# Kernel optimization log

Measured on AMD Instinct MI355X. Metric: run time of the kernel, lower is better.

Reference implementation:

```python
import jax, jax.numpy as jnp
import numpy as np

B, H, W, DIM, NH = 4, 32, 32, 768, 12
HD = DIM // NH  # head_dim = 64


def setup_inputs() -> dict:
    key = jax.random.key(0)
    ks = jax.random.split(key, 12)
    n = lambda i, shape, s=1.0: jax.random.normal(ks[i], shape, jnp.float32) * s
    return {
        "q": n(0, (B, H, W, DIM)),
        "k": n(1, (B, H, W, DIM)),
        "v": n(2, (B, H, W, DIM)),
        # Linear weights stored as (in, out) so y = x @ W + b (equivalent to torch x @ W.T)
        "Wq": n(3, (DIM, DIM), 0.02), "bq": jnp.zeros((DIM,), jnp.float32),
        "Wk": n(4, (DIM, DIM), 0.02), "bk": jnp.zeros((DIM,), jnp.float32),
        "Wv": n(5, (DIM, DIM), 0.02), "bv": jnp.zeros((DIM,), jnp.float32),
        "Wp": n(6, (DIM, DIM), 0.02), "bp": jnp.zeros((DIM,), jnp.float32),
        # decomposed relative position tables: (2*size - 1, head_dim)
        "rel_pos_h": n(7, (2 * H - 1, HD), 0.02),
        "rel_pos_w": n(8, (2 * W - 1, HD), 0.02),
    }


def reference(q, k, v, Wq, bq, Wk, bk, Wv, bv, Wp, bp, rel_pos_h, rel_pos_w):
    scale = HD ** -0.5

    def to_heads(x, Wt, b):
        y = x.reshape(B, H * W, DIM) @ Wt + b          # (B, HW, DIM)
        return y.reshape(B, H * W, NH, HD).transpose(0, 2, 1, 3).reshape(B * NH, H * W, HD)

    qh = to_heads(q, Wq, bq)   # (B*NH, HW, HD)
    kh = to_heads(k, Wk, bk)
    vh = to_heads(v, Wv, bv)

    # scaled dot-product scores
    attn = jnp.einsum('bqd,bkd->bqk', qh * scale, kh)  # (B*NH, HW, HW)

    # decomposed relative position bias (q_size == k_size == input_size, no interpolation)
    idx_h = jnp.arange(H)[:, None] - jnp.arange(H)[None, :] + (H - 1)
    idx_w = jnp.arange(W)[:, None] - jnp.arange(W)[None, :] + (W - 1)
    Rh = rel_pos_h[idx_h]  # (H, H, HD)
    Rw = rel_pos_w[idx_w]  # (W, W, HD)
    rq = qh.reshape(B * NH, H, W, HD)  # unscaled q, as in torch add_decomposed_rel_pos
    rel_h = jnp.einsum('bhwc,hkc->bhwk', rq, Rh)  # (B*NH, H, W, H)
    rel_w = jnp.einsum('bhwc,wkc->bhwk', rq, Rw)  # (B*NH, H, W, W)

    attn = (attn.reshape(B * NH, H, W, H, W)
            + rel_h[:, :, :, :, None]
            + rel_w[:, :, :, None, :]).reshape(B * NH, H * W, H * W)

    attn = jax.nn.softmax(attn, axis=-1)
    x = (attn @ vh).reshape(B, NH, H, W, HD).transpose(0, 2, 3, 1, 4).reshape(B, H, W, DIM)
    return x @ Wp + bp
```

## Files before the change

### kernel.cpp

```cpp
#include <hip/hip_runtime.h>
#include <math.h>

#define DIM  768
#define NH   12
#define HD   64
#define HWN  1024
#define MROWS 4096

typedef __attribute__((ext_vector_type(8))) short short8;
typedef __attribute__((ext_vector_type(4))) float f32x4;
typedef _Float16 h8 __attribute__((ext_vector_type(8)));
typedef _Float16 h2 __attribute__((ext_vector_type(2)));

__device__ __forceinline__ void gl_lds16(const void* g, void* l) {
    __builtin_amdgcn_global_load_lds(
        (const __attribute__((address_space(1))) void*)g,
        (__attribute__((address_space(3))) void*)l, 16, 0, 0);
}

__global__ __launch_bounds__(256) void xconv_kernel(
    const float* __restrict__ q, const float* __restrict__ k,
    const float* __restrict__ v, _Float16* __restrict__ xf16)
{
    const int N8 = MROWS * DIM / 8;
    int i = blockIdx.x * 256 + threadIdx.x;
    const int stride = gridDim.x * 256;
    for (; i < 3 * N8; i += stride) {
        const int sel = i / N8, j = i - sel * N8;
        const float* src = (sel == 0) ? q : (sel == 1) ? k : v;
        float4 a0 = ((const float4*)src)[j * 2];
        float4 a1 = ((const float4*)src)[j * 2 + 1];
        h8 o = {(_Float16)a0.x, (_Float16)a0.y, (_Float16)a0.z, (_Float16)a0.w,
                (_Float16)a1.x, (_Float16)a1.y, (_Float16)a1.z, (_Float16)a1.w};
        *(h8*)(xf16 + (size_t)sel * (MROWS * DIM) + (size_t)j * 8) = o;
    }
}

__global__ __launch_bounds__(256) void wconv_kernel(
    const float* __restrict__ Wq, const float* __restrict__ Wk,
    const float* __restrict__ Wv, const float* __restrict__ Wp,
    _Float16* __restrict__ WtAll)
{
    __shared__ float Ws[64][65];
    const int z = blockIdx.z;
    const float* W = (z == 0) ? Wq : (z == 1) ? Wk : (z == 2) ? Wv : Wp;
    _Float16* Wt = WtAll + (size_t)z * 589824;

    const int k0 = blockIdx.y * 64, n0 = blockIdx.x * 64;
    const int t = threadIdx.x;
    {
        int r = t >> 2, c4 = (t & 3) * 16;
        #pragma unroll
        for (int u = 0; u < 16; u += 4)
            *(float4*)&Ws[r][c4 + u] = *(const float4*)(W + (size_t)(k0 + r) * DIM + n0 + c4 + u);
    }
    __syncthreads();
    const int n = t >> 2, kseg = (t & 3) * 16;
    h8 h0, h1;
    #pragma unroll
    for (int j = 0; j < 8; ++j) {
        h0[j] = (_Float16)Ws[kseg + j][n];
        h1[j] = (_Float16)Ws[kseg + 8 + j][n];
    }
    size_t base = (size_t)(n0 + n) * DIM + k0 + kseg;
    *(h8*)(Wt + base) = h0;
    *(h8*)(Wt + base + 8) = h1;
}

__global__ __launch_bounds__(256) void rel2frag_kernel(
    const float* __restrict__ rph, const float* __restrict__ rpw,
    _Float16* __restrict__ relTg)
{
    const int t = threadIdx.x;
    const int row = t >> 1, c0 = (t & 1) * 32;
    const float* src = (row < 63) ? rph + (size_t)row * HD
                     : (row >= 64 && row < 127) ? rpw + (size_t)(row - 64) * HD
                     : nullptr;
    #pragma unroll
    for (int g = 0; g < 4; ++g) {
        h8 o;
        #pragma unroll
        for (int j = 0; j < 8; ++j)
            o[j] = src ? (_Float16)src[c0 + g * 8 + j] : (_Float16)0.0f;
        *(h8*)(relTg + (size_t)row * HD + c0 + g * 8) = o;
    }
}

template<int AMODE>
__global__ __launch_bounds__(256, 3) void gemm_mfma_kernel(
    const _Float16* __restrict__ X0, const _Float16* __restrict__ WtAll,
    const float* __restrict__ bias0, const float* __restrict__ bias1,
    const float* __restrict__ bias2,
    void* __restrict__ Y0, void* __restrict__ Y1, void* __restrict__ Y2)
{
    constexpr int NT  = (AMODE == 0) ? 128 : 64;
    constexpr int NBF = NT / 16;
    constexpr int WCF = NT / 32;
    __shared__ __align__(16) char smem[16384 + 2 * NBF * 1024];
    constexpr int BOFF = 16384;

    const int t = threadIdx.x;
    const int w = t >> 6, lane = t & 63;
    const int l15 = lane & 15, l4 = lane >> 4;

    int sel, rem, rb, cb;
    if (AMODE == 0) {
        const int sw = (blockIdx.x & 7) * 72 + (blockIdx.x >> 3);
        sel = sw / 192; rem = sw - sel * 192;
        rb = rem / 6; cb = rem - rb * 6;
    } else {
        const int sw = (blockIdx.x & 7) * 48 + (blockIdx.x >> 3);
        sel = 3; rem = sw;
        rb = rem / 12; cb = rem - rb * 12;
    }
    const int row0 = rb * 128, col0 = cb * NT;

    const char* Ab = (const char*)(X0 + (AMODE == 0 ? (size_t)sel * (MROWS * DIM) : 0));
    const _Float16* Bt = WtAll + (size_t)sel * 589824;
    const float* bias = (AMODE == 1) ? bias0 : (sel == 0) ? bias0 : (sel == 1) ? bias1 : bias2;

    f32x4 acc[4][WCF];
    #pragma unroll
    for (int i = 0; i < 4; ++i)
        #pragma unroll
        for (int j = 0; j < WCF; ++j) acc[i][j] = (f32x4){0, 0, 0, 0};

    for (int kt = 0; kt < 12; ++kt) {
        #pragma unroll
        for (int i = 0; i < 4; ++i) {
            const int fi = w * 4 + i;
            const int row = fi * 8 + (lane >> 3);
            const int srcb = ((lane & 7) * 16) ^ ((row & 7) << 4);
            gl_lds16(Ab + (size_t)(row0 + row) * 1536 + kt * 128 + srcb, smem + fi * 1024);
        }
        #pragma unroll
        for (int it = 0; it < 2 * NBF / 4; ++it) {
            const int f = it * 4 + w;
            const int ks = f / NBF, cf = f % NBF;
            const size_t off = (size_t)(col0 + cf * 16 + l15) * 1536 + kt * 128 + ks * 64 + l4 * 16;
            gl_lds16((const char*)Bt + off, smem + BOFF + f * 1024);
        }
        __syncthreads();

        __builtin_amdgcn_s_setprio(1);
        #pragma unroll
        for (int ks = 0; ks < 2; ++ks) {
            h8 b[WCF];
            #pragma unroll
            for (int cf4 = 0; cf4 < WCF; ++cf4) {
                const int fb = ks * NBF + (w & 1) * WCF + cf4;
                b[cf4] = *(const h8*)(smem + BOFF + fb * 1024 + lane * 16);
            }
            #pragma unroll
            for (int rf = 0; rf < 4; ++rf) {
                const int arow = (w >> 1) * 64 + rf * 16 + l15;
                const int base = arow * 128 + ((ks * 64 + l4 * 16) ^ ((arow & 7) << 4));
                h8 ah = *(const h8*)(smem + base);
                #pragma unroll
                for (int cf4 = 0; cf4 < WCF; ++cf4)
                    acc[rf][cf4] = __builtin_amdgcn_mfma_f32_16x16x32_f16(ah, b[cf4], acc[rf][cf4], 0, 0, 0);
            }
        }
        __builtin_amdgcn_s_setprio(0);
        __syncthreads();
    }

    const int wrow0 = row0 + (w >> 1) * 64;
    const int wcol0 = col0 + (w & 1) * (WCF * 16);
    #pragma unroll
    for (int cf4 = 0; cf4 < WCF; ++cf4) {
        const int c = wcol0 + cf4 * 16 + l15;
        const float bb = bias[c - (AMODE == 0 ? 0 : col0) + (AMODE == 0 ? 0 : col0)];
        #pragma unroll
        for (int rf = 0; rf < 4; ++rf) {
            #pragma unroll
            for (int reg = 0; reg < 4; ++reg) {
                const int r = wrow0 + rf * 16 + l4 * 4 + reg;
                float y = acc[rf][cf4][reg] + bb;
                if (AMODE == 1) {
                    ((float*)Y0)[(size_t)r * DIM + c] = y;
                } else {
                    _Float16* Yh = (_Float16*)((sel == 0) ? Y0 : (sel == 1) ? Y1 : Y2);
                    size_t base = ((size_t)((r >> 10) * NH + (c >> 6)) * HWN + (r & 1023)) * HD + (c & 63);
                    Yh[base] = (_Float16)y;
                }
            }
        }
    }
}

#define AT_REL   0
#define AT_VT    8704
#define AT_P     25088
#define AT_KB    33280
#define AT_QF    8704
#define AT_RELT  17920
#define AT_PG    17920
#define AT_OF    8704
#define AT_TOTAL 49664

__global__ __launch_bounds__(256, 3) void attn_kernel(
    const _Float16* __restrict__ qh, const _Float16* __restrict__ kh,
    const _Float16* __restrict__ vh, const _Float16* __restrict__ relTg,
    _Float16* __restrict__ aout)
{
    __shared__ __align__(16) char smem[AT_TOTAL];
    const int bid = blockIdx.x;
    const int j   = bid >> 3;
    const int bh  = (bid & 7) * 6 + (j >> 4);
    const int qb  = j & 15;
    const int t  = threadIdx.x;
    const int w  = t >> 6;
    const int lane = t & 63;
    const int l15 = lane & 15, l4 = lane >> 4;

    _Float16* Rel = (_Float16*)(smem + AT_REL);
    _Float16* Qf  = (_Float16*)(smem + AT_QF);

    const int r = t >> 2, dc = (t & 3) * 16;
    {
        const _Float16* qp = qh + ((size_t)bh * HWN + qb * 64 + r) * HD + dc;
        *(short8*)(&Qf[r * 72 + dc])     = *(const short8*)(qp);
        *(short8*)(&Qf[r * 72 + dc + 8]) = *(const short8*)(qp + 8);
        #pragma unroll
        for (int it = 0; it < 4; ++it) {
            const int f = it * 4 + w;
            const int ct = f >> 1, ks = f & 1;
            gl_lds16((const char*)relTg + (ct * 16 + l15) * 128 + ks * 64 + l4 * 16,
                     smem + AT_RELT + f * 1024);
        }
    }
    __syncthreads();

    const _Float16* kb_ = kh + (size_t)bh * HWN * HD;
    const _Float16* vb_ = vh + (size_t)bh * HWN * HD;
    const int key2 = (t & 31) * 2, dgrp = t >> 5;
    short8 rv0, rv1;
#define LOADV(KT) {                                                            \
        const _Float16* vp = vb_ + (size_t)((KT) * 64 + key2) * HD + dgrp * 8; \
        rv0 = *(const short8*)vp; rv1 = *(const short8*)(vp + HD); }
    LOADV(0);

    h8 qf2[2];
    {
        const int qr = w * 16 + l15;
        qf2[0] = *(const h8*)(&Qf[qr * 72 + l4 * 8]);
        qf2[1] = *(const h8*)(&Qf[qr * 72 + 32 + l4 * 8]);
        #pragma unroll
        for (int j2 = 0; j2 < 8; ++j2) { qf2[0][j2] *= (_Float16)0.125f; qf2[1][j2] *= (_Float16)0.125f; }
    }

    f32x4 pacc[4][2];
    #pragma unroll
    for (int i = 0; i < 4; ++i)
        #pragma unroll
        for (int j2 = 0; j2 < 2; ++j2) pacc[i][j2] = (f32x4){0, 0, 0, 0};
    #pragma unroll
    for (int ks = 0; ks < 2; ++ks) {
        h8 b0 = *(const h8*)(smem + AT_RELT + ((w * 2 + 0) * 2 + ks) * 1024 + lane * 16);
        h8 b1 = *(const h8*)(smem + AT_RELT + ((w * 2 + 1) * 2 + ks) * 1024 + lane * 16);
        #pragma unroll
        for (int rt = 0; rt < 4; ++rt) {
            h8 a = *(const h8*)(&Qf[(rt * 16 + l15) * 72 + ks * 32 + l4 * 8]);
            pacc[rt][0] = __builtin_amdgcn_mfma_f32_16x16x32_f16(a, b0, pacc[rt][0], 0, 0, 0);
            pacc[rt][1] = __builtin_amdgcn_mfma_f32_16x16x32_f16(a, b1, pacc[rt][1], 0, 0, 0);
        }
    }

    __syncthreads();
    _Float16* Pg = (_Float16*)(smem + AT_PG);
    #pragma unroll
    for (int rt = 0; rt < 4; ++rt)
        #pragma unroll
        for (int cb2 = 0; cb2 < 2; ++cb2)
            #pragma unroll
            for (int reg = 0; reg < 4; ++reg)
                Pg[(rt * 16 + l4 * 4 + reg) * 130 + w * 32 + cb2 * 16 + l15] =
                    (_Float16)pacc[rt][cb2][reg];
    __syncthreads();

    {
        const int q = t >> 2, kk0 = (t & 3) * 8;
        const int hw = qb * 64 + q;
        const int hq = hw >> 5, wq = hw & 31;
        short8 vh_, vw_;
        #pragma unroll
        for (int j2 = 0; j2 < 8; ++j2) {
            const int kk = kk0 + j2;
            vh_[j2] = *(const short*)&Pg[q * 130 + (hq + 31 - kk)];
            vw_[j2] = *(const short*)&Pg[q * 130 + 64 + (wq + 31 - kk)];
        }
        *(short8*)(&Rel[q * 68 + kk0])      = vh_;
        *(short8*)(&Rel[q * 68 + 32 + kk0]) = vw_;
    }
    __syncthreads();

    const int qrow_bias = w * 16 + l15;
    float rw_[2][4];
    #pragma unroll
    for (int c2 = 0; c2 < 2; ++c2)
        #pragma unroll
        for (int reg = 0; reg < 4; ++reg)
            rw_[c2][reg] = (float)Rel[qrow_bias * 68 + 32 + c2 * 16 + l4 * 4 + reg];

#define STAGEK(KT, BUF) {                                                      \
        _Pragma("unroll")                                                      \
        for (int i2 = 0; i2 < 2; ++i2) {                                       \
            const int f = w * 2 + i2;                                          \
            const int keyk = f * 8 + (lane >> 3);                              \
            const int srcb = ((lane & 7) * 16) ^ ((lane >> 3) << 4);           \
            gl_lds16((const char*)kb_ + (size_t)((KT) * 64 + keyk) * 128 + srcb, \
                     smem + AT_KB + (BUF) * 8192 + f * 1024);                  \
        } }

#define WRITEVT(BUF) {                                                         \
        _Pragma("unroll")                                                      \
        for (int j2 = 0; j2 < 8; ++j2) {                                       \
            const int d = dgrp * 8 + j2;                                       \
            unsigned pk = ((unsigned short)rv0[j2]) |                          \
                          (((unsigned)(unsigned short)rv1[j2]) << 16);         \
            *(unsigned*)(smem + AT_VT + (BUF) * 8192 + d * 128 +               \
                         ((key2 * 2) ^ ((d & 7) << 4))) = pk; } }
    WRITEVT(0);
    STAGEK(0, 0);

    f32x4 acc_o[4] = {{0,0,0,0},{0,0,0,0},{0,0,0,0},{0,0,0,0}};
    float m_ = -INFINITY, l_ = 0.f;
    char* Pw = smem + AT_P + w * 2048;
    const int swzP = (l15 & 7) << 4;

    #pragma unroll 2
    for (int kt = 0; kt < 16; ++kt) {
        const int cur = kt & 1;
        __syncthreads();
        if (kt < 15) { LOADV(kt + 1); STAGEK(kt + 1, cur ^ 1); }

        const float rh0 = (float)Rel[qrow_bias * 68 + kt * 2];
        const float rh1 = (float)Rel[qrow_bias * 68 + kt * 2 + 1];
        f32x4 accs[4];
        #pragma unroll
        for (int ct = 0; ct < 4; ++ct) {
            const float rhc = (ct >> 1) ? rh1 : rh0;
            #pragma unroll
            for (int reg = 0; reg < 4; ++reg)
                accs[ct][reg] = rw_[ct & 1][reg] + rhc;
        }
        __builtin_amdgcn_s_setprio(1);
        #pragma unroll
        for (int ct = 0; ct < 4; ++ct) {
            const int row = ct * 16 + l15;
            const int swzK = (row & 7) << 4;
            #pragma unroll
            for (int ks = 0; ks < 2; ++ks) {
                h8 kfr = *(const h8*)(smem + AT_KB + cur * 8192 + row * 128 +
                                      ((ks * 64 + l4 * 16) ^ swzK));
                accs[ct] = __builtin_amdgcn_mfma_f32_16x16x32_f16(kfr, qf2[ks], accs[ct], 0, 0, 0);
            }
        }
        __builtin_amdgcn_s_setprio(0);

        float mx[4];
        #pragma unroll
        for (int ct = 0; ct < 4; ++ct)
            mx[ct] = fmaxf(fmaxf(accs[ct][0], accs[ct][1]),
                           fmaxf(accs[ct][2], accs[ct][3]));
        float tmax = fmaxf(fmaxf(mx[0], mx[1]), fmaxf(mx[2], mx[3]));
        tmax = fmaxf(tmax, __shfl_xor(tmax, 16));
        tmax = fmaxf(tmax, __shfl_xor(tmax, 32));

        if (__any(tmax > m_ + 8.f)) {
            const float mnew = fmaxf(m_, tmax);
            const float factor = __expf(m_ - mnew);
            m_ = mnew;
            l_ *= factor;
            #pragma unroll
            for (int reg = 0; reg < 4; ++reg) {
                const float fr = __shfl(factor, l4 * 4 + reg);
                #pragma unroll
                for (int dt = 0; dt < 4; ++dt) acc_o[dt][reg] *= fr;
            }
        }

        float tsum = 0.f;
        #pragma unroll
        for (int ct = 0; ct < 4; ++ct) {
            float p0 = __expf(accs[ct][0] - m_);
            float p1 = __expf(accs[ct][1] - m_);
            float p2 = __expf(accs[ct][2] - m_);
            float p3 = __expf(accs[ct][3] - m_);
            tsum += (p0 + p1) + (p2 + p3);
            h2 pa = {(_Float16)p0, (_Float16)p1};
            h2 pb = {(_Float16)p2, (_Float16)p3};
            uint2 pk;
            pk.x = *(unsigned*)&pa;
            pk.y = *(unsigned*)&pb;
            *(uint2*)(Pw + l15 * 128 + ((ct * 32 + l4 * 8) ^ swzP)) = pk;
        }
        tsum += __shfl_xor(tsum, 16);
        tsum += __shfl_xor(tsum, 32);
        l_ += tsum;

        __builtin_amdgcn_s_setprio(1);
        #pragma unroll
        for (int ks = 0; ks < 2; ++ks) {
            h8 pa = *(const h8*)(Pw + l15 * 128 + ((ks * 64 + l4 * 16) ^ swzP));
            #pragma unroll
            for (int dt = 0; dt < 4; ++dt) {
                const int d = dt * 16 + l15;
                h8 vf = *(const h8*)(smem + AT_VT + cur * 8192 + d * 128 +
                                     ((ks * 64 + l4 * 16) ^ ((d & 7) << 4)));
                acc_o[dt] = __builtin_amdgcn_mfma_f32_16x16x32_f16(pa, vf, acc_o[dt], 0, 0, 0);
            }
        }
        __builtin_amdgcn_s_setprio(0);

        if (kt < 15) WRITEVT(cur ^ 1);
    }

    const float invl = 1.0f / l_;
    float linv[4];
    #pragma unroll
    for (int reg = 0; reg < 4; ++reg) linv[reg] = __shfl(invl, l4 * 4 + reg);
    __syncthreads();
    _Float16* Of = (_Float16*)(smem + AT_OF);
    #pragma unroll
    for (int reg = 0; reg < 4; ++reg) {
        const int qloc = w * 16 + l4 * 4 + reg;
        #pragma unroll
        for (int dt = 0; dt < 4; ++dt)
            Of[qloc * 72 + dt * 16 + l15] = (_Float16)(acc_o[dt][reg] * linv[reg]);
    }
    __syncthreads();
    {
        const int b_ = bh / NH, nh = bh % NH;
        _Float16* op = aout + ((size_t)b_ * HWN + qb * 64 + r) * DIM + nh * HD + dc;
        *(short8*)op       = *(const short8*)(&Of[r * 72 + dc]);
        *(short8*)(op + 8) = *(const short8*)(&Of[r * 72 + dc + 8]);
    }
}

extern "C" void kernel_launch(void* const* d_in, const int* in_sizes, int n_in,
                              void* d_out, int out_size, void* d_ws, size_t ws_size,
                              hipStream_t stream) {
    const float* q   = (const float*)d_in[0];
    const float* k   = (const float*)d_in[1];
    const float* v   = (const float*)d_in[2];
    const float* Wq  = (const float*)d_in[3];
    const float* bq  = (const float*)d_in[4];
    const float* Wk  = (const float*)d_in[5];
    const float* bk  = (const float*)d_in[6];
    const float* Wv  = (const float*)d_in[7];
    const float* bv  = (const float*)d_in[8];
    const float* Wp  = (const float*)d_in[9];
    const float* bp  = (const float*)d_in[10];
    const float* rph = (const float*)d_in[11];
    const float* rpw = (const float*)d_in[12];

    float* out = (float*)d_out;
    char*  w0  = (char*)d_ws;

    _Float16* wtAll = (_Float16*)(w0);
    _Float16* relTg = (_Float16*)(w0 + 4718592);
    _Float16* xf16  = (_Float16*)(w0 + 4734976);
    _Float16* aout  = (_Float16*)(w0 + 4734976);
    _Float16* qf16  = (_Float16*)(w0 + 23609344);
    _Float16* kf16  = (_Float16*)(w0 + 29900800);
    _Float16* vf16  = (_Float16*)(w0 + 36192256);

    dim3 blk(256);
    xconv_kernel<<<2048, blk, 0, stream>>>(q, k, v, xf16);
    wconv_kernel<<<dim3(12, 12, 4), blk, 0, stream>>>(Wq, Wk, Wv, Wp, wtAll);
    rel2frag_kernel<<<1, blk, 0, stream>>>(rph, rpw, relTg);
    gemm_mfma_kernel<0><<<576, blk, 0, stream>>>(
        xf16, wtAll, bq, bk, bv, qf16, kf16, vf16);
    attn_kernel<<<768, blk, 0, stream>>>(qf16, kf16, vf16, relTg, aout);
    gemm_mfma_kernel<1><<<384, blk, 0, stream>>>(
        aout, wtAll, bp, nullptr, nullptr, out, nullptr, nullptr);
}
```

Before: 100.3 us.

## Retile projection GEMMs to 96-wide columns and defer softmax row-sum reduction

The QKV GEMM moves from 128x128 tiles to 128x96, and the output projection from 128x64 to 64x96. This raises block counts to 768 and 512 so the workload spreads more evenly across the MI355X CUs. In the attention kernel, the per-tile cross-lane row-sum shuffles are dropped: each lane keeps a partial sum and reduces once at the end, and the max shuffles now happen only inside the rescale branch. The relative-height bias pair is read with one packed half2 load instead of two scalar loads. Deferring the sum relies on every lane in a row sharing the same running max, and the narrower tiles lower per-block reuse of the A operand.

```diff
diff --git a/kernel.cpp b/kernel.cpp
--- a/kernel.cpp
+++ b/kernel.cpp
@@ -93,50 +93,50 @@
     const float* __restrict__ bias2,
     void* __restrict__ Y0, void* __restrict__ Y1, void* __restrict__ Y2)
 {
-    constexpr int NT  = (AMODE == 0) ? 128 : 64;
-    constexpr int NBF = NT / 16;
-    constexpr int WCF = NT / 32;
-    __shared__ __align__(16) char smem[16384 + 2 * NBF * 1024];
-    constexpr int BOFF = 16384;
+    constexpr int MT = (AMODE == 0) ? 128 : 64;
+    constexpr int RF = MT / 32;
+    __shared__ __align__(16) char smem[MT * 128 + 12 * 1024];
+    constexpr int BOFF = MT * 128;
 
     const int t = threadIdx.x;
     const int w = t >> 6, lane = t & 63;
     const int l15 = lane & 15, l4 = lane >> 4;
 
-    int sel, rem, rb, cb;
+    int sel, rb, cb;
     if (AMODE == 0) {
-        const int sw = (blockIdx.x & 7) * 72 + (blockIdx.x >> 3);
-        sel = sw / 192; rem = sw - sel * 192;
-        rb = rem / 6; cb = rem - rb * 6;
+        const int sw = (blockIdx.x & 7) * 96 + (blockIdx.x >> 3);
+        sel = sw >> 8;
+        const int rem = sw & 255;
+        rb = rem >> 3; cb = rem & 7;
     } else {
-        const int sw = (blockIdx.x & 7) * 48 + (blockIdx.x >> 3);
-        sel = 3; rem = sw;
-        rb = rem / 12; cb = rem - rb * 12;
-    }
-    const int row0 = rb * 128, col0 = cb * NT;
+        const int sw = (blockIdx.x & 7) * 64 + (blockIdx.x >> 3);
+        sel = 3;
+        rb = sw >> 3; cb = sw & 7;
+    }
+    const int row0 = rb * MT, col0 = cb * 96;
 
     const char* Ab = (const char*)(X0 + (AMODE == 0 ? (size_t)sel * (MROWS * DIM) : 0));
     const _Float16* Bt = WtAll + (size_t)sel * 589824;
     const float* bias = (AMODE == 1) ? bias0 : (sel == 0) ? bias0 : (sel == 1) ? bias1 : bias2;
 
-    f32x4 acc[4][WCF];
-    #pragma unroll
-    for (int i = 0; i < 4; ++i)
-        #pragma unroll
-        for (int j = 0; j < WCF; ++j) acc[i][j] = (f32x4){0, 0, 0, 0};
+    f32x4 acc[RF][3];
+    #pragma unroll
+    for (int i = 0; i < RF; ++i)
+        #pragma unroll
+        for (int j = 0; j < 3; ++j) acc[i][j] = (f32x4){0, 0, 0, 0};
 
     for (int kt = 0; kt < 12; ++kt) {
         #pragma unroll
-        for (int i = 0; i < 4; ++i) {
-            const int fi = w * 4 + i;
+        for (int i = 0; i < MT / 32; ++i) {
+            const int fi = w * (MT / 32) + i;
             const int row = fi * 8 + (lane >> 3);
             const int srcb = ((lane & 7) * 16) ^ ((row & 7) << 4);
             gl_lds16(Ab + (size_t)(row0 + row) * 1536 + kt * 128 + srcb, smem + fi * 1024);
         }
         #pragma unroll
-        for (int it = 0; it < 2 * NBF / 4; ++it) {
+        for (int it = 0; it < 3; ++it) {
             const int f = it * 4 + w;
-            const int ks = f / NBF, cf = f % NBF;
+            const int ks = f / 6, cf = f % 6;
             const size_t off = (size_t)(col0 + cf * 16 + l15) * 1536 + kt * 128 + ks * 64 + l4 * 16;
             gl_lds16((const char*)Bt + off, smem + BOFF + f * 1024);
         }
@@ -145,19 +145,19 @@
         __builtin_amdgcn_s_setprio(1);
         #pragma unroll
         for (int ks = 0; ks < 2; ++ks) {
-            h8 b[WCF];
-            #pragma unroll
-            for (int cf4 = 0; cf4 < WCF; ++cf4) {
-                const int fb = ks * NBF + (w & 1) * WCF + cf4;
+            h8 b[3];
+            #pragma unroll
+            for (int cf4 = 0; cf4 < 3; ++cf4) {
+                const int fb = ks * 6 + (w & 1) * 3 + cf4;
                 b[cf4] = *(const h8*)(smem + BOFF + fb * 1024 + lane * 16);
             }
             #pragma unroll
-            for (int rf = 0; rf < 4; ++rf) {
-                const int arow = (w >> 1) * 64 + rf * 16 + l15;
+            for (int rf = 0; rf < RF; ++rf) {
+                const int arow = (w >> 1) * (MT / 2) + rf * 16 + l15;
                 const int base = arow * 128 + ((ks * 64 + l4 * 16) ^ ((arow & 7) << 4));
                 h8 ah = *(const h8*)(smem + base);
                 #pragma unroll
-                for (int cf4 = 0; cf4 < WCF; ++cf4)
+                for (int cf4 = 0; cf4 < 3; ++cf4)
                     acc[rf][cf4] = __builtin_amdgcn_mfma_f32_16x16x32_f16(ah, b[cf4], acc[rf][cf4], 0, 0, 0);
             }
         }
@@ -165,14 +165,14 @@
         __syncthreads();
     }
 
-    const int wrow0 = row0 + (w >> 1) * 64;
-    const int wcol0 = col0 + (w & 1) * (WCF * 16);
-    #pragma unroll
-    for (int cf4 = 0; cf4 < WCF; ++cf4) {
+    const int wrow0 = row0 + (w >> 1) * (MT / 2);
+    const int wcol0 = col0 + (w & 1) * 48;
+    #pragma unroll
+    for (int cf4 = 0; cf4 < 3; ++cf4) {
         const int c = wcol0 + cf4 * 16 + l15;
-        const float bb = bias[c - (AMODE == 0 ? 0 : col0) + (AMODE == 0 ? 0 : col0)];
-        #pragma unroll
-        for (int rf = 0; rf < 4; ++rf) {
+        const float bb = bias[c];
+        #pragma unroll
+        for (int rf = 0; rf < RF; ++rf) {
             #pragma unroll
             for (int reg = 0; reg < 4; ++reg) {
                 const int r = wrow0 + rf * 16 + l4 * 4 + reg;
@@ -325,7 +325,7 @@
     STAGEK(0, 0);
 
     f32x4 acc_o[4] = {{0,0,0,0},{0,0,0,0},{0,0,0,0},{0,0,0,0}};
-    float m_ = -INFINITY, l_ = 0.f;
+    float m_ = -INFINITY, lsum = 0.f;
     char* Pw = smem + AT_P + w * 2048;
     const int swzP = (l15 & 7) << 4;
 
@@ -335,8 +335,9 @@
         __syncthreads();
         if (kt < 15) { LOADV(kt + 1); STAGEK(kt + 1, cur ^ 1); }
 
-        const float rh0 = (float)Rel[qrow_bias * 68 + kt * 2];
-        const float rh1 = (float)Rel[qrow_bias * 68 + kt * 2 + 1];
+        h2 rhp = *(const h2*)(&Rel[qrow_bias * 68 + kt * 2]);
+        const float rh0 = (float)rhp[0];
+        const float rh1 = (float)rhp[1];
         f32x4 accs[4];
         #pragma unroll
         for (int ct = 0; ct < 4; ++ct) {
@@ -365,14 +366,14 @@
             mx[ct] = fmaxf(fmaxf(accs[ct][0], accs[ct][1]),
                            fmaxf(accs[ct][2], accs[ct][3]));
         float tmax = fmaxf(fmaxf(mx[0], mx[1]), fmaxf(mx[2], mx[3]));
-        tmax = fmaxf(tmax, __shfl_xor(tmax, 16));
-        tmax = fmaxf(tmax, __shfl_xor(tmax, 32));
 
         if (__any(tmax > m_ + 8.f)) {
-            const float mnew = fmaxf(m_, tmax);
+            float tg = fmaxf(tmax, __shfl_xor(tmax, 16));
+            tg = fmaxf(tg, __shfl_xor(tg, 32));
+            const float mnew = fmaxf(m_, tg);
             const float factor = __expf(m_ - mnew);
             m_ = mnew;
-            l_ *= factor;
+            lsum *= factor;
             #pragma unroll
             for (int reg = 0; reg < 4; ++reg) {
                 const float fr = __shfl(factor, l4 * 4 + reg);
@@ -396,9 +397,7 @@
             pk.y = *(unsigned*)&pb;
             *(uint2*)(Pw + l15 * 128 + ((ct * 32 + l4 * 8) ^ swzP)) = pk;
         }
-        tsum += __shfl_xor(tsum, 16);
-        tsum += __shfl_xor(tsum, 32);
-        l_ += tsum;
+        lsum += tsum;
 
         __builtin_amdgcn_s_setprio(1);
         #pragma unroll
@@ -417,7 +416,9 @@
         if (kt < 15) WRITEVT(cur ^ 1);
     }
 
-    const float invl = 1.0f / l_;
+    float ltot = lsum + __shfl_xor(lsum, 16);
+    ltot += __shfl_xor(ltot, 32);
+    const float invl = 1.0f / ltot;
     float linv[4];
     #pragma unroll
     for (int reg = 0; reg < 4; ++reg) linv[reg] = __shfl(invl, l4 * 4 + reg);
@@ -471,9 +472,9 @@
     xconv_kernel<<<2048, blk, 0, stream>>>(q, k, v, xf16);
     wconv_kernel<<<dim3(12, 12, 4), blk, 0, stream>>>(Wq, Wk, Wv, Wp, wtAll);
     rel2frag_kernel<<<1, blk, 0, stream>>>(rph, rpw, relTg);
-    gemm_mfma_kernel<0><<<576, blk, 0, stream>>>(
+    gemm_mfma_kernel<0><<<768, blk, 0, stream>>>(
         xf16, wtAll, bq, bk, bv, qf16, kf16, vf16);
     attn_kernel<<<768, blk, 0, stream>>>(qf16, kf16, vf16, relTg, aout);
-    gemm_mfma_kernel<1><<<384, blk, 0, stream>>>(
+    gemm_mfma_kernel<1><<<512, blk, 0, stream>>>(
         aout, wtAll, bp, nullptr, nullptr, out, nullptr, nullptr);
 }
```

After: 95.12 us. -5.2%, faster.
